# Optimization experiments

Measured on AMD Instinct MI355X. Metric: run time of the kernel, lower is better.

Reference implementation:

```python
import jax, jax.numpy as jnp
import numpy as np

EMBED_DIM = 128
NUM_HEADS = 4
WINDOW = 7
L = WINDOW * WINDOW  # 49 tokens per window
D_K = EMBED_DIM // NUM_HEADS
NUM_WINDOWS = 1024   # windows per image (224/7)^2
B_TOTAL = 8192       # image_batch(8) * NUM_WINDOWS


def _relative_position_index(window):
    ch, cw = np.meshgrid(np.arange(window), np.arange(window), indexing='ij')
    coords = np.stack([ch.ravel(), cw.ravel()])              # [2, L]
    rel = coords[:, :, None] - coords[:, None, :]            # [2, L, L]
    rel = rel.transpose(1, 2, 0)                             # [L, L, 2]
    rel[:, :, 0] += window - 1
    rel[:, :, 1] += window - 1
    rel[:, :, 0] *= 2 * window - 1
    return rel.sum(-1)                                       # [L, L] int

REL_IDX = jnp.asarray(_relative_position_index(WINDOW))


def setup_inputs() -> dict:
    key = jax.random.key(0)
    ks = jax.random.split(key, 8)
    q = jax.random.normal(ks[0], (B_TOTAL, L, EMBED_DIM), jnp.float32)
    k = jax.random.normal(ks[1], (B_TOTAL, L, EMBED_DIM), jnp.float32)
    v = jax.random.normal(ks[2], (B_TOTAL, L, EMBED_DIM), jnp.float32)
    # shift-mask style additive mask (0 / -100 pattern emulated by random floats is less
    # faithful; build a real 0/-100 mask from a random window partition)
    mkey = jax.random.fold_in(key, 99)
    groups = jax.random.randint(mkey, (NUM_WINDOWS, L), 0, 4)
    mask = jnp.where(groups[:, :, None] == groups[:, None, :], 0.0, -100.0).astype(jnp.float32)
    Wq = jax.random.normal(ks[3], (EMBED_DIM, EMBED_DIM), jnp.float32) * 0.02
    Wk = jax.random.normal(ks[4], (EMBED_DIM, EMBED_DIM), jnp.float32) * 0.02
    Wv = jax.random.normal(ks[5], (EMBED_DIM, EMBED_DIM), jnp.float32) * 0.02
    Wo = jax.random.normal(ks[6], (EMBED_DIM, EMBED_DIM), jnp.float32) * 0.02
    bo = jnp.zeros((EMBED_DIM,), jnp.float32)
    rel_table = jax.random.normal(ks[7], ((2 * WINDOW - 1) ** 2, NUM_HEADS), jnp.float32) * 0.02
    return {"q": q, "k": k, "v": v, "mask": mask, "Wq": Wq, "Wk": Wk,
            "Wv": Wv, "Wo": Wo, "bo": bo, "rel_table": rel_table}


def reference(q, k, v, mask, Wq, Wk, Wv, Wo, bo, rel_table):
    B = q.shape[0]
    # linear projections (torch Linear: x @ W.T), split heads -> [B, H, L, d]
    def proj(x, W):
        return (x @ W.T).reshape(B, L, NUM_HEADS, D_K).transpose(0, 2, 1, 3)
    qh, kh, vh = proj(q, Wq), proj(k, Wk), proj(v, Wv)

    energy = jnp.einsum('bhld,bhmd->bhlm', qh, kh) / jnp.sqrt(jnp.float32(D_K))
    # gathered relative position bias: [L, L, H] -> [1, H, L, L]
    bias = rel_table[REL_IDX].transpose(2, 0, 1)[None]
    energy = energy + bias
    # additive shift mask per window: [B//nW, nW, H, L, L] + mask[None,:,None]
    nW = mask.shape[0]
    energy = energy.reshape(-1, nW, NUM_HEADS, L, L) + mask[None, :, None]
    energy = energy.reshape(B, NUM_HEADS, L, L)

    attn = jax.nn.softmax(energy, axis=-1)
    out = jnp.einsum('bhlm,bhmd->bhld', attn, vh)
    out = out.transpose(0, 2, 1, 3).reshape(B, L, EMBED_DIM)
    return out @ Wo.T + bo
```

## Files before the change

kernel.cpp:

```cpp
#include <hip/hip_runtime.h>

#define TOK 49
#define DIM 128
#define NHEAD 4
#define NWIN 1024
#define SCALE 0.17677669529663687f

typedef __bf16 bf16x8 __attribute__((ext_vector_type(8)));
typedef short s16x4 __attribute__((ext_vector_type(4)));
typedef float f32x4 __attribute__((ext_vector_type(4)));
typedef unsigned short u16;
typedef unsigned int u32;

#if defined(__HIP_DEVICE_COMPILE__)
#define MFMA16(a, b, c) __builtin_amdgcn_mfma_f32_16x16x16bf16_1k(a, b, c, 0, 0, 0)
#define MFMA32(a, b, c) __builtin_amdgcn_mfma_f32_16x16x32_bf16(a, b, c, 0, 0, 0)
#else
__device__ inline f32x4 MFMA16(s16x4, s16x4, f32x4 c) { return c; }
__device__ inline f32x4 MFMA32(bf16x8, bf16x8, f32x4 c) { return c; }
#endif

__device__ __forceinline__ int xo256(int row, int kbyte) {
    return row * 256 + (kbyte ^ ((row & 7) << 4));
}
__device__ __forceinline__ u16 bfbits(float x) {
    __bf16 t = (__bf16)x;
    return __builtin_bit_cast(u16, t);
}
__device__ __forceinline__ float bf2f(u16 x) {
    u32 u = ((u32)x) << 16;
    return __builtin_bit_cast(float, u);
}
__device__ __forceinline__ bf16x8 cvt8(const float* __restrict__ p) {
    float4 a = *reinterpret_cast<const float4*>(p);
    float4 bq = *reinterpret_cast<const float4*>(p + 4);
    bf16x8 r;
    r[0] = (__bf16)a.x; r[1] = (__bf16)a.y; r[2] = (__bf16)a.z; r[3] = (__bf16)a.w;
    r[4] = (__bf16)bq.x; r[5] = (__bf16)bq.y; r[6] = (__bf16)bq.z; r[7] = (__bf16)bq.w;
    return r;
}
__device__ __forceinline__ bf16x8 cvt8s(const float* __restrict__ p, float s) {
    float4 a = *reinterpret_cast<const float4*>(p);
    float4 bq = *reinterpret_cast<const float4*>(p + 4);
    bf16x8 r;
    r[0] = (__bf16)(a.x * s); r[1] = (__bf16)(a.y * s);
    r[2] = (__bf16)(a.z * s); r[3] = (__bf16)(a.w * s);
    r[4] = (__bf16)(bq.x * s); r[5] = (__bf16)(bq.y * s);
    r[6] = (__bf16)(bq.z * s); r[7] = (__bf16)(bq.w * s);
    return r;
}
__device__ __forceinline__ s16x4 pack4(const f32x4& a) {
    s16x4 r;
    r[0] = (short)bfbits(a[0]); r[1] = (short)bfbits(a[1]);
    r[2] = (short)bfbits(a[2]); r[3] = (short)bfbits(a[3]);
    return r;
}
__device__ __forceinline__ s16x4 pack4s(const f32x4& a, float s) {
    s16x4 r;
    r[0] = (short)bfbits(a[0] * s); r[1] = (short)bfbits(a[1] * s);
    r[2] = (short)bfbits(a[2] * s); r[3] = (short)bfbits(a[3] * s);
    return r;
}

__global__ void fused_pre_kernel(const float* __restrict__ mask, const float* __restrict__ rel,
                                 u16* __restrict__ tbl) {
    const int idx = blockIdx.x * 256 + threadIdx.x;
    const int w = idx >> 14, h = (idx >> 12) & 3, l = (idx >> 6) & 63, m = idx & 63;
    float v = 0.0f;
    if (l < TOK && m < TOK) {
        const int dl = l / 7 - m / 7 + 6;
        const int dc = l % 7 - m % 7 + 6;
        v = mask[(w * TOK + l) * TOK + m] + rel[(dl * 13 + dc) * NHEAD + h];
    }
    tbl[idx] = bfbits(v);
}

__global__ void bias_pre_kernel(const float* __restrict__ rel, float* __restrict__ biasT) {
    const int idx = blockIdx.x * 256 + threadIdx.x;
    const int h = idx >> 12, l = (idx >> 6) & 63, m = idx & 63;
    float v = 0.0f;
    if (l < TOK && m < TOK) {
        const int dl = l / 7 - m / 7 + 6;
        const int dc = l % 7 - m % 7 + 6;
        v = rel[(dl * 13 + dc) * NHEAD + h];
    }
    biasT[idx] = v;
}

__global__ void wcvt_kernel(const float* __restrict__ Wq, const float* __restrict__ Wk,
                            const float* __restrict__ Wv, const float* __restrict__ Wo,
                            u16* __restrict__ tbl) {
    const int idx = blockIdx.x * 256 + threadIdx.x;
    const int mat = idx >> 14, e = idx & 16383;
    float v;
    if (mat == 0)      v = Wq[e] * SCALE;
    else if (mat == 1) v = Wk[e];
    else if (mat == 2) v = Wv[e];
    else               v = Wo[e];
    tbl[idx] = bfbits(v);
}

template <int MODE>
__global__ __launch_bounds__(256, 3) void winattn_kernel(
    const float* __restrict__ q, const float* __restrict__ k, const float* __restrict__ v,
    const float* __restrict__ mask, const float* __restrict__ Wq, const float* __restrict__ Wk,
    const float* __restrict__ Wv, const float* __restrict__ Wo, const float* __restrict__ bo,
    const u16* __restrict__ wtbl, const u16* __restrict__ fmtbl, const float* __restrict__ btbl,
    float* __restrict__ out)
{
    __shared__ __align__(16) char LA[16384];
    __shared__ __align__(16) char LB[16384];
    const int tid = threadIdx.x;
    const int wave = tid >> 6;
    const int lane = tid & 63;
    const int l16 = lane & 15;
    const int k8 = lane >> 4;
    const int b = blockIdx.x;
    const int h = wave;

    const float* qp = q + (size_t)b * (TOK * DIM);
    const float* kp = k + (size_t)b * (TOK * DIM);
    const float* vp = v + (size_t)b * (TOK * DIM);
    float* op = out + (size_t)b * (TOK * DIM);

    auto ldw = [&](int mat, int row, int kk) -> bf16x8 {
        return *reinterpret_cast<const bf16x8*>(
            reinterpret_cast<const __bf16*>(wtbl) + (mat << 14) + row * DIM + kk * 32 + k8 * 8);
    };
    auto ldx = [&](const char* buf, int row, int kk) -> bf16x8 {
        return *reinterpret_cast<const bf16x8*>(buf + xo256(row, kk * 64 + k8 * 16));
    };

    float4 tv[8];
    {
        float4 t[8];
        #pragma unroll
        for (int p = 0; p < 8; ++p) {
            const int idx = p * 256 + tid;
            const int row = idx >> 5;
            const int c4 = (idx & 31) * 4;
            t[p] = (row < TOK) ? *reinterpret_cast<const float4*>(qp + row * DIM + c4)
                               : float4{0.f, 0.f, 0.f, 0.f};
        }
        #pragma unroll
        for (int p = 0; p < 8; ++p) {
            const int idx = p * 256 + tid;
            uint2 pq;
            pq.x = (u32)bfbits(t[p].x) | ((u32)bfbits(t[p].y) << 16);
            pq.y = (u32)bfbits(t[p].z) | ((u32)bfbits(t[p].w) << 16);
            *reinterpret_cast<uint2*>(LA + xo256(idx >> 5, (idx & 31) * 8)) = pq;
        }
        #pragma unroll
        for (int p = 0; p < 8; ++p) {
            const int idx = p * 256 + tid;
            const int row = idx >> 5;
            const int c4 = (idx & 31) * 4;
            t[p] = (row < TOK) ? *reinterpret_cast<const float4*>(kp + row * DIM + c4)
                               : float4{0.f, 0.f, 0.f, 0.f};
        }
        #pragma unroll
        for (int p = 0; p < 8; ++p) {
            const int idx = p * 256 + tid;
            const int row = idx >> 5;
            const int c4 = (idx & 31) * 4;
            tv[p] = (row < TOK) ? *reinterpret_cast<const float4*>(vp + row * DIM + c4)
                                : float4{0.f, 0.f, 0.f, 0.f};
        }
        #pragma unroll
        for (int p = 0; p < 8; ++p) {
            const int idx = p * 256 + tid;
            uint2 pk2;
            pk2.x = (u32)bfbits(t[p].x) | ((u32)bfbits(t[p].y) << 16);
            pk2.y = (u32)bfbits(t[p].z) | ((u32)bfbits(t[p].w) << 16);
            *reinterpret_cast<uint2*>(LB + xo256(idx >> 5, (idx & 31) * 8)) = pk2;
        }
    }
    __syncthreads();

    uint2 pv[8];
    #pragma unroll
    for (int p = 0; p < 8; ++p) {
        pv[p].x = (u32)bfbits(tv[p].x) | ((u32)bfbits(tv[p].y) << 16);
        pv[p].y = (u32)bfbits(tv[p].z) | ((u32)bfbits(tv[p].w) << 16);
    }

    s16x4 qf[2][4], kf[2][4];
    {
        f32x4 acc[2][4];
        #pragma unroll
        for (int t = 0; t < 2; ++t)
            #pragma unroll
            for (int ni = 0; ni < 4; ++ni) acc[t][ni] = f32x4{0.f, 0.f, 0.f, 0.f};
        #pragma unroll
        for (int kk = 0; kk < 4; ++kk) {
            bf16x8 wa[2], xb[4];
            #pragma unroll
            for (int t = 0; t < 2; ++t)
                wa[t] = (MODE == 0) ? ldw(0, h * 32 + t * 16 + l16, kk)
                                    : cvt8s(Wq + (h * 32 + t * 16 + l16) * DIM + kk * 32 + k8 * 8, SCALE);
            #pragma unroll
            for (int ni = 0; ni < 4; ++ni) xb[ni] = ldx(LA, ni * 16 + l16, kk);
            #pragma unroll
            for (int t = 0; t < 2; ++t)
                #pragma unroll
                for (int ni = 0; ni < 4; ++ni) acc[t][ni] = MFMA32(wa[t], xb[ni], acc[t][ni]);
        }
        #pragma unroll
        for (int t = 0; t < 2; ++t)
            #pragma unroll
            for (int ni = 0; ni < 4; ++ni) qf[t][ni] = pack4(acc[t][ni]);
    }
    {
        f32x4 acc[2][4];
        #pragma unroll
        for (int t = 0; t < 2; ++t)
            #pragma unroll
            for (int mi = 0; mi < 4; ++mi) acc[t][mi] = f32x4{0.f, 0.f, 0.f, 0.f};
        #pragma unroll
        for (int kk = 0; kk < 4; ++kk) {
            bf16x8 wa[2], xb[4];
            #pragma unroll
            for (int t = 0; t < 2; ++t)
                wa[t] = (MODE == 0) ? ldw(1, h * 32 + t * 16 + l16, kk)
                                    : cvt8(Wk + (h * 32 + t * 16 + l16) * DIM + kk * 32 + k8 * 8);
            #pragma unroll
            for (int mi = 0; mi < 4; ++mi) xb[mi] = ldx(LB, mi * 16 + l16, kk);
            #pragma unroll
            for (int t = 0; t < 2; ++t)
                #pragma unroll
                for (int mi = 0; mi < 4; ++mi) acc[t][mi] = MFMA32(wa[t], xb[mi], acc[t][mi]);
        }
        #pragma unroll
        for (int t = 0; t < 2; ++t)
            #pragma unroll
            for (int mi = 0; mi < 4; ++mi) kf[t][mi] = pack4(acc[t][mi]);
    }
    __syncthreads();

    #pragma unroll
    for (int p = 0; p < 8; ++p) {
        const int idx = p * 256 + tid;
        *reinterpret_cast<uint2*>(LA + xo256(idx >> 5, (idx & 31) * 8)) = pv[p];
    }
    __syncthreads();

    s16x4 pf[4][4];
    {
        const u16* frow = (MODE == 0)
            ? fmtbl + ((((size_t)(b & (NWIN - 1)) * NHEAD) + h) << 12) : nullptr;
        const float* brow = (MODE == 1) ? btbl + ((size_t)h << 12) : nullptr;
        const float* mp = mask + (size_t)(b & (NWIN - 1)) * (TOK * TOK);
        #pragma unroll
        for (int ni = 0; ni < 4; ++ni) {
            f32x4 ec[4];
            #pragma unroll
            for (int mi = 0; mi < 4; ++mi) {
                f32x4 c = {0.f, 0.f, 0.f, 0.f};
                c = MFMA16(kf[0][mi], qf[0][ni], c);
                ec[mi] = MFMA16(kf[1][mi], qf[1][ni], c);
            }
            const int l = ni * 16 + l16;
            const bool lv = l < TOK;
            #pragma unroll
            for (int mi = 0; mi < 4; ++mi) {
                const int m0 = mi * 16 + k8 * 4;
                float ad[4];
                if constexpr (MODE == 0) {
                    const uint2 raw = *reinterpret_cast<const uint2*>(frow + l * 64 + m0);
                    ad[0] = bf2f((u16)(raw.x & 0xffffu));
                    ad[1] = bf2f((u16)(raw.x >> 16));
                    ad[2] = bf2f((u16)(raw.y & 0xffffu));
                    ad[3] = bf2f((u16)(raw.y >> 16));
                } else {
                    const float4 bg = *reinterpret_cast<const float4*>(brow + l * 64 + m0);
                    ad[0] = bg.x; ad[1] = bg.y; ad[2] = bg.z; ad[3] = bg.w;
                    #pragma unroll
                    for (int r = 0; r < 4; ++r) {
                        const int m = m0 + r;
                        if (lv && m < TOK) ad[r] += mp[l * TOK + m];
                    }
                }
                #pragma unroll
                for (int r = 0; r < 4; ++r) {
                    const int m = m0 + r;
                    ec[mi][r] = (lv && m < TOK) ? ec[mi][r] + ad[r] : -1e30f;
                }
            }
            float mx = -1e30f;
            #pragma unroll
            for (int mi = 0; mi < 4; ++mi)
                #pragma unroll
                for (int r = 0; r < 4; ++r) mx = fmaxf(mx, ec[mi][r]);
            mx = fmaxf(mx, __shfl_xor(mx, 16));
            mx = fmaxf(mx, __shfl_xor(mx, 32));
            float s = 0.f;
            #pragma unroll
            for (int mi = 0; mi < 4; ++mi) {
                #pragma unroll
                for (int r = 0; r < 4; ++r) {
                    const float p = __expf(ec[mi][r] - mx);
                    ec[mi][r] = p;
                    s += p;
                }
            }
            s += __shfl_xor(s, 16);
            s += __shfl_xor(s, 32);
            const float rs = 1.0f / s;
            #pragma unroll
            for (int mi = 0; mi < 4; ++mi) pf[mi][ni] = pack4s(ec[mi], rs);
        }
    }

    s16x4 vf[4][2];
    {
        f32x4 acc[4][2];
        #pragma unroll
        for (int mi = 0; mi < 4; ++mi)
            #pragma unroll
            for (int nn = 0; nn < 2; ++nn) acc[mi][nn] = f32x4{0.f, 0.f, 0.f, 0.f};
        #pragma unroll
        for (int kk = 0; kk < 4; ++kk) {
            bf16x8 xa[4], wb[2];
            #pragma unroll
            for (int mi = 0; mi < 4; ++mi) xa[mi] = ldx(LA, mi * 16 + l16, kk);
            #pragma unroll
            for (int nn = 0; nn < 2; ++nn)
                wb[nn] = (MODE == 0) ? ldw(2, h * 32 + nn * 16 + l16, kk)
                                     : cvt8(Wv + (h * 32 + nn * 16 + l16) * DIM + kk * 32 + k8 * 8);
            #pragma unroll
            for (int mi = 0; mi < 4; ++mi)
                #pragma unroll
                for (int nn = 0; nn < 2; ++nn) acc[mi][nn] = MFMA32(xa[mi], wb[nn], acc[mi][nn]);
        }
        #pragma unroll
        for (int mi = 0; mi < 4; ++mi)
            #pragma unroll
            for (int nn = 0; nn < 2; ++nn) vf[mi][nn] = pack4(acc[mi][nn]);
    }

    f32x4 o_[4][2];
    #pragma unroll
    for (int ni = 0; ni < 4; ++ni) {
        #pragma unroll
        for (int nn = 0; nn < 2; ++nn) {
            f32x4 c = {0.f, 0.f, 0.f, 0.f};
            #pragma unroll
            for (int mi = 0; mi < 4; ++mi) c = MFMA16(pf[mi][ni], vf[mi][nn], c);
            o_[ni][nn] = c;
        }
    }

    #pragma unroll
    for (int ni = 0; ni < 4; ++ni) {
        #pragma unroll
        for (int nn = 0; nn < 2; ++nn) {
            const int d = h * 32 + nn * 16 + l16;
            #pragma unroll
            for (int r = 0; r < 4; ++r) {
                const int row = ni * 16 + k8 * 4 + r;
                *reinterpret_cast<u16*>(LB + xo256(row, d * 2)) = bfbits(o_[ni][nn][r]);
            }
        }
    }
    bf16x8 aw[2][4];
    #pragma unroll
    for (int m2 = 0; m2 < 2; ++m2) {
        const int o = (wave * 2 + m2) * 16 + l16;
        #pragma unroll
        for (int kk = 0; kk < 4; ++kk)
            aw[m2][kk] = (MODE == 0) ? ldw(3, o, kk)
                                     : cvt8(Wo + o * DIM + kk * 32 + k8 * 8);
    }
    __syncthreads();

    #pragma unroll
    for (int ni = 0; ni < 4; ++ni) {
        const int l = ni * 16 + l16;
        bf16x8 bx[4];
        #pragma unroll
        for (int kk = 0; kk < 4; ++kk)
            bx[kk] = *reinterpret_cast<const bf16x8*>(LB + xo256(l, kk * 64 + k8 * 16));
        #pragma unroll
        for (int m2 = 0; m2 < 2; ++m2) {
            f32x4 c = {0.f, 0.f, 0.f, 0.f};
            #pragma unroll
            for (int kk = 0; kk < 4; ++kk) c = MFMA32(aw[m2][kk], bx[kk], c);
            if (l < TOK) {
                const int o0 = (wave * 2 + m2) * 16 + k8 * 4;
                const float4 bias = *reinterpret_cast<const float4*>(bo + o0);
                float4 st;
                st.x = c[0] + bias.x;
                st.y = c[1] + bias.y;
                st.z = c[2] + bias.z;
                st.w = c[3] + bias.w;
                *reinterpret_cast<float4*>(op + l * DIM + o0) = st;
            }
        }
    }
}

extern "C" void kernel_launch(void* const* d_in, const int* in_sizes, int n_in,
                              void* d_out, int out_size, void* d_ws, size_t ws_size,
                              hipStream_t stream) {
    const float* q    = (const float*)d_in[0];
    const float* k    = (const float*)d_in[1];
    const float* v    = (const float*)d_in[2];
    const float* mask = (const float*)d_in[3];
    const float* Wq   = (const float*)d_in[4];
    const float* Wk   = (const float*)d_in[5];
    const float* Wv   = (const float*)d_in[6];
    const float* Wo   = (const float*)d_in[7];
    const float* bo   = (const float*)d_in[8];
    const float* rel  = (const float*)d_in[9];
    float* out = (float*)d_out;

    const int B = in_sizes[0] / (TOK * DIM);
    const size_t FUSED_BYTES = (size_t)NWIN * NHEAD * 64 * 64 * sizeof(u16);
    const size_t W_BYTES     = (size_t)4 * DIM * DIM * sizeof(u16);
    const size_t BIAS_BYTES  = (size_t)NHEAD * 64 * 64 * sizeof(float);

    if (ws_size >= FUSED_BYTES + W_BYTES) {
        u16* fmtbl = (u16*)d_ws;
        u16* wtbl  = (u16*)((char*)d_ws + FUSED_BYTES);
        fused_pre_kernel<<<dim3(NWIN * NHEAD * 64 * 64 / 256), dim3(256), 0, stream>>>(
            mask, rel, fmtbl);
        wcvt_kernel<<<dim3(4 * DIM * DIM / 256), dim3(256), 0, stream>>>(Wq, Wk, Wv, Wo, wtbl);
        winattn_kernel<0><<<dim3(B), dim3(256), 0, stream>>>(q, k, v, mask, Wq, Wk, Wv, Wo,
                                                             bo, wtbl, fmtbl, nullptr, out);
    } else {
        float* btbl = (float*)d_ws;
        bias_pre_kernel<<<dim3(NHEAD * 64 * 64 / 256), dim3(256), 0, stream>>>(rel, btbl);
        winattn_kernel<1><<<dim3(B), dim3(256), 0, stream>>>(q, k, v, mask, Wq, Wk, Wv, Wo,
                                                             bo, nullptr, nullptr, btbl, out);
    }
}
```

Before: 337.5 us.

## Process two windows per block and prefetch next window's Q during output stage

Each block now handles two consecutive windows in a loop. It prefetches the next window's Q into registers while the current window's output projection runs, and issues the K/V loads earlier. The fused bias/mask table entries are also loaded into registers ahead of the softmax rather than inline. This aims to hide global-load latency with compute, at the cost of higher register pressure and half as many blocks in the grid.

```diff
diff --git a/kernel.cpp b/kernel.cpp
--- a/kernel.cpp
+++ b/kernel.cpp
@@ -106,7 +106,7 @@
     const float* __restrict__ mask, const float* __restrict__ Wq, const float* __restrict__ Wk,
     const float* __restrict__ Wv, const float* __restrict__ Wo, const float* __restrict__ bo,
     const u16* __restrict__ wtbl, const u16* __restrict__ fmtbl, const float* __restrict__ btbl,
-    float* __restrict__ out)
+    float* __restrict__ out, int btot)
 {
     __shared__ __align__(16) char LA[16384];
     __shared__ __align__(16) char LB[16384];
@@ -115,13 +115,8 @@
     const int lane = tid & 63;
     const int l16 = lane & 15;
     const int k8 = lane >> 4;
-    const int b = blockIdx.x;
+    const int b0 = blockIdx.x * 2;
     const int h = wave;
-
-    const float* qp = q + (size_t)b * (TOK * DIM);
-    const float* kp = k + (size_t)b * (TOK * DIM);
-    const float* vp = v + (size_t)b * (TOK * DIM);
-    float* op = out + (size_t)b * (TOK * DIM);
 
     auto ldw = [&](int mat, int row, int kk) -> bf16x8 {
         return *reinterpret_cast<const bf16x8*>(
@@ -130,272 +125,280 @@
     auto ldx = [&](const char* buf, int row, int kk) -> bf16x8 {
         return *reinterpret_cast<const bf16x8*>(buf + xo256(row, kk * 64 + k8 * 16));
     };
-
-    float4 tv[8];
-    {
-        float4 t[8];
+    auto gload = [&](float4* dst, const float* __restrict__ src) {
         #pragma unroll
         for (int p = 0; p < 8; ++p) {
             const int idx = p * 256 + tid;
             const int row = idx >> 5;
             const int c4 = (idx & 31) * 4;
-            t[p] = (row < TOK) ? *reinterpret_cast<const float4*>(qp + row * DIM + c4)
-                               : float4{0.f, 0.f, 0.f, 0.f};
-        }
-        #pragma unroll
-        for (int p = 0; p < 8; ++p) {
-            const int idx = p * 256 + tid;
-            uint2 pq;
-            pq.x = (u32)bfbits(t[p].x) | ((u32)bfbits(t[p].y) << 16);
-            pq.y = (u32)bfbits(t[p].z) | ((u32)bfbits(t[p].w) << 16);
-            *reinterpret_cast<uint2*>(LA + xo256(idx >> 5, (idx & 31) * 8)) = pq;
-        }
-        #pragma unroll
-        for (int p = 0; p < 8; ++p) {
-            const int idx = p * 256 + tid;
-            const int row = idx >> 5;
-            const int c4 = (idx & 31) * 4;
-            t[p] = (row < TOK) ? *reinterpret_cast<const float4*>(kp + row * DIM + c4)
-                               : float4{0.f, 0.f, 0.f, 0.f};
-        }
-        #pragma unroll
-        for (int p = 0; p < 8; ++p) {
-            const int idx = p * 256 + tid;
-            const int row = idx >> 5;
-            const int c4 = (idx & 31) * 4;
-            tv[p] = (row < TOK) ? *reinterpret_cast<const float4*>(vp + row * DIM + c4)
-                                : float4{0.f, 0.f, 0.f, 0.f};
-        }
+            dst[p] = (row < TOK) ? *reinterpret_cast<const float4*>(src + row * DIM + c4)
+                                 : float4{0.f, 0.f, 0.f, 0.f};
+        }
+    };
+    auto lwrite = [&](char* L, const float4* src) {
         #pragma unroll
         for (int p = 0; p < 8; ++p) {
             const int idx = p * 256 + tid;
             uint2 pk2;
-            pk2.x = (u32)bfbits(t[p].x) | ((u32)bfbits(t[p].y) << 16);
-            pk2.y = (u32)bfbits(t[p].z) | ((u32)bfbits(t[p].w) << 16);
-            *reinterpret_cast<uint2*>(LB + xo256(idx >> 5, (idx & 31) * 8)) = pk2;
-        }
-    }
-    __syncthreads();
-
-    uint2 pv[8];
-    #pragma unroll
-    for (int p = 0; p < 8; ++p) {
-        pv[p].x = (u32)bfbits(tv[p].x) | ((u32)bfbits(tv[p].y) << 16);
-        pv[p].y = (u32)bfbits(tv[p].z) | ((u32)bfbits(tv[p].w) << 16);
-    }
-
-    s16x4 qf[2][4], kf[2][4];
-    {
-        f32x4 acc[2][4];
-        #pragma unroll
-        for (int t = 0; t < 2; ++t)
-            #pragma unroll
-            for (int ni = 0; ni < 4; ++ni) acc[t][ni] = f32x4{0.f, 0.f, 0.f, 0.f};
-        #pragma unroll
-        for (int kk = 0; kk < 4; ++kk) {
-            bf16x8 wa[2], xb[4];
-            #pragma unroll
-            for (int t = 0; t < 2; ++t)
-                wa[t] = (MODE == 0) ? ldw(0, h * 32 + t * 16 + l16, kk)
-                                    : cvt8s(Wq + (h * 32 + t * 16 + l16) * DIM + kk * 32 + k8 * 8, SCALE);
-            #pragma unroll
-            for (int ni = 0; ni < 4; ++ni) xb[ni] = ldx(LA, ni * 16 + l16, kk);
-            #pragma unroll
-            for (int t = 0; t < 2; ++t)
-                #pragma unroll
-                for (int ni = 0; ni < 4; ++ni) acc[t][ni] = MFMA32(wa[t], xb[ni], acc[t][ni]);
-        }
-        #pragma unroll
-        for (int t = 0; t < 2; ++t)
-            #pragma unroll
-            for (int ni = 0; ni < 4; ++ni) qf[t][ni] = pack4(acc[t][ni]);
-    }
-    {
-        f32x4 acc[2][4];
-        #pragma unroll
-        for (int t = 0; t < 2; ++t)
-            #pragma unroll
-            for (int mi = 0; mi < 4; ++mi) acc[t][mi] = f32x4{0.f, 0.f, 0.f, 0.f};
-        #pragma unroll
-        for (int kk = 0; kk < 4; ++kk) {
-            bf16x8 wa[2], xb[4];
-            #pragma unroll
-            for (int t = 0; t < 2; ++t)
-                wa[t] = (MODE == 0) ? ldw(1, h * 32 + t * 16 + l16, kk)
-                                    : cvt8(Wk + (h * 32 + t * 16 + l16) * DIM + kk * 32 + k8 * 8);
-            #pragma unroll
-            for (int mi = 0; mi < 4; ++mi) xb[mi] = ldx(LB, mi * 16 + l16, kk);
-            #pragma unroll
-            for (int t = 0; t < 2; ++t)
-                #pragma unroll
-                for (int mi = 0; mi < 4; ++mi) acc[t][mi] = MFMA32(wa[t], xb[mi], acc[t][mi]);
-        }
-        #pragma unroll
-        for (int t = 0; t < 2; ++t)
-            #pragma unroll
-            for (int mi = 0; mi < 4; ++mi) kf[t][mi] = pack4(acc[t][mi]);
-    }
-    __syncthreads();
-
-    #pragma unroll
-    for (int p = 0; p < 8; ++p) {
-        const int idx = p * 256 + tid;
-        *reinterpret_cast<uint2*>(LA + xo256(idx >> 5, (idx & 31) * 8)) = pv[p];
-    }
-    __syncthreads();
-
-    s16x4 pf[4][4];
-    {
-        const u16* frow = (MODE == 0)
-            ? fmtbl + ((((size_t)(b & (NWIN - 1)) * NHEAD) + h) << 12) : nullptr;
-        const float* brow = (MODE == 1) ? btbl + ((size_t)h << 12) : nullptr;
-        const float* mp = mask + (size_t)(b & (NWIN - 1)) * (TOK * TOK);
-        #pragma unroll
-        for (int ni = 0; ni < 4; ++ni) {
-            f32x4 ec[4];
-            #pragma unroll
-            for (int mi = 0; mi < 4; ++mi) {
-                f32x4 c = {0.f, 0.f, 0.f, 0.f};
-                c = MFMA16(kf[0][mi], qf[0][ni], c);
-                ec[mi] = MFMA16(kf[1][mi], qf[1][ni], c);
-            }
-            const int l = ni * 16 + l16;
-            const bool lv = l < TOK;
-            #pragma unroll
-            for (int mi = 0; mi < 4; ++mi) {
-                const int m0 = mi * 16 + k8 * 4;
-                float ad[4];
-                if constexpr (MODE == 0) {
-                    const uint2 raw = *reinterpret_cast<const uint2*>(frow + l * 64 + m0);
-                    ad[0] = bf2f((u16)(raw.x & 0xffffu));
-                    ad[1] = bf2f((u16)(raw.x >> 16));
-                    ad[2] = bf2f((u16)(raw.y & 0xffffu));
-                    ad[3] = bf2f((u16)(raw.y >> 16));
-                } else {
-                    const float4 bg = *reinterpret_cast<const float4*>(brow + l * 64 + m0);
-                    ad[0] = bg.x; ad[1] = bg.y; ad[2] = bg.z; ad[3] = bg.w;
+            pk2.x = (u32)bfbits(src[p].x) | ((u32)bfbits(src[p].y) << 16);
+            pk2.y = (u32)bfbits(src[p].z) | ((u32)bfbits(src[p].w) << 16);
+            *reinterpret_cast<uint2*>(L + xo256(idx >> 5, (idx & 31) * 8)) = pk2;
+        }
+    };
+
+    float4 t[8];
+    gload(t, q + (size_t)b0 * (TOK * DIM));
+
+    #pragma unroll 1
+    for (int it = 0; it < 2; ++it) {
+        const int b = b0 + it;
+        if (b >= btot) break;
+        const float* kp = k + (size_t)b * (TOK * DIM);
+        const float* vp = v + (size_t)b * (TOK * DIM);
+        float* op = out + (size_t)b * (TOK * DIM);
+
+        lwrite(LA, t);
+        float4 tv[8];
+        gload(t, kp);
+        gload(tv, vp);
+        __syncthreads();
+
+        s16x4 qf[2][4], kf[2][4];
+        {
+            f32x4 acc[2][4];
+            #pragma unroll
+            for (int t2 = 0; t2 < 2; ++t2)
+                #pragma unroll
+                for (int ni = 0; ni < 4; ++ni) acc[t2][ni] = f32x4{0.f, 0.f, 0.f, 0.f};
+            #pragma unroll
+            for (int kk = 0; kk < 4; ++kk) {
+                bf16x8 wa[2], xb[4];
+                #pragma unroll
+                for (int t2 = 0; t2 < 2; ++t2)
+                    wa[t2] = (MODE == 0) ? ldw(0, h * 32 + t2 * 16 + l16, kk)
+                                         : cvt8s(Wq + (h * 32 + t2 * 16 + l16) * DIM + kk * 32 + k8 * 8, SCALE);
+                #pragma unroll
+                for (int ni = 0; ni < 4; ++ni) xb[ni] = ldx(LA, ni * 16 + l16, kk);
+                #pragma unroll
+                for (int t2 = 0; t2 < 2; ++t2)
+                    #pragma unroll
+                    for (int ni = 0; ni < 4; ++ni) acc[t2][ni] = MFMA32(wa[t2], xb[ni], acc[t2][ni]);
+            }
+            #pragma unroll
+            for (int t2 = 0; t2 < 2; ++t2)
+                #pragma unroll
+                for (int ni = 0; ni < 4; ++ni) qf[t2][ni] = pack4(acc[t2][ni]);
+        }
+
+        lwrite(LB, t);
+        uint2 pv[8];
+        #pragma unroll
+        for (int p = 0; p < 8; ++p) {
+            pv[p].x = (u32)bfbits(tv[p].x) | ((u32)bfbits(tv[p].y) << 16);
+            pv[p].y = (u32)bfbits(tv[p].z) | ((u32)bfbits(tv[p].w) << 16);
+        }
+        __syncthreads();
+
+        uint2 tbl[16];
+        if constexpr (MODE == 0) {
+            const u16* frow = fmtbl + ((((size_t)(b & (NWIN - 1)) * NHEAD) + h) << 12);
+            #pragma unroll
+            for (int ni = 0; ni < 4; ++ni) {
+                const int l = ni * 16 + l16;
+                #pragma unroll
+                for (int mi = 0; mi < 4; ++mi)
+                    tbl[ni * 4 + mi] = *reinterpret_cast<const uint2*>(
+                        frow + l * 64 + mi * 16 + k8 * 4);
+            }
+        }
+
+        {
+            f32x4 acc[2][4];
+            #pragma unroll
+            for (int t2 = 0; t2 < 2; ++t2)
+                #pragma unroll
+                for (int mi = 0; mi < 4; ++mi) acc[t2][mi] = f32x4{0.f, 0.f, 0.f, 0.f};
+            #pragma unroll
+            for (int kk = 0; kk < 4; ++kk) {
+                bf16x8 wa[2], xb[4];
+                #pragma unroll
+                for (int t2 = 0; t2 < 2; ++t2)
+                    wa[t2] = (MODE == 0) ? ldw(1, h * 32 + t2 * 16 + l16, kk)
+                                         : cvt8(Wk + (h * 32 + t2 * 16 + l16) * DIM + kk * 32 + k8 * 8);
+                #pragma unroll
+                for (int mi = 0; mi < 4; ++mi) xb[mi] = ldx(LB, mi * 16 + l16, kk);
+                #pragma unroll
+                for (int t2 = 0; t2 < 2; ++t2)
+                    #pragma unroll
+                    for (int mi = 0; mi < 4; ++mi) acc[t2][mi] = MFMA32(wa[t2], xb[mi], acc[t2][mi]);
+            }
+            #pragma unroll
+            for (int t2 = 0; t2 < 2; ++t2)
+                #pragma unroll
+                for (int mi = 0; mi < 4; ++mi) kf[t2][mi] = pack4(acc[t2][mi]);
+        }
+
+        #pragma unroll
+        for (int p = 0; p < 8; ++p) {
+            const int idx = p * 256 + tid;
+            *reinterpret_cast<uint2*>(LA + xo256(idx >> 5, (idx & 31) * 8)) = pv[p];
+        }
+        __syncthreads();
+
+        s16x4 pf[4][4];
+        {
+            const float* brow = (MODE == 1) ? btbl + ((size_t)h << 12) : nullptr;
+            const float* mp = mask + (size_t)(b & (NWIN - 1)) * (TOK * TOK);
+            #pragma unroll
+            for (int ni = 0; ni < 4; ++ni) {
+                f32x4 ec[4];
+                #pragma unroll
+                for (int mi = 0; mi < 4; ++mi) {
+                    f32x4 c = {0.f, 0.f, 0.f, 0.f};
+                    c = MFMA16(kf[0][mi], qf[0][ni], c);
+                    ec[mi] = MFMA16(kf[1][mi], qf[1][ni], c);
+                }
+                const int l = ni * 16 + l16;
+                const bool lv = l < TOK;
+                #pragma unroll
+                for (int mi = 0; mi < 4; ++mi) {
+                    const int m0 = mi * 16 + k8 * 4;
+                    float ad[4];
+                    if constexpr (MODE == 0) {
+                        const uint2 raw = tbl[ni * 4 + mi];
+                        ad[0] = bf2f((u16)(raw.x & 0xffffu));
+                        ad[1] = bf2f((u16)(raw.x >> 16));
+                        ad[2] = bf2f((u16)(raw.y & 0xffffu));
+                        ad[3] = bf2f((u16)(raw.y >> 16));
+                    } else {
+                        const float4 bg = *reinterpret_cast<const float4*>(brow + l * 64 + m0);
+                        ad[0] = bg.x; ad[1] = bg.y; ad[2] = bg.z; ad[3] = bg.w;
+                        #pragma unroll
+                        for (int r = 0; r < 4; ++r) {
+                            const int m = m0 + r;
+                            if (lv && m < TOK) ad[r] += mp[l * TOK + m];
+                        }
+                    }
                     #pragma unroll
                     for (int r = 0; r < 4; ++r) {
                         const int m = m0 + r;
-                        if (lv && m < TOK) ad[r] += mp[l * TOK + m];
+                        ec[mi][r] = (lv && m < TOK) ? ec[mi][r] + ad[r] : -1e30f;
                     }
                 }
+                float mx = -1e30f;
+                #pragma unroll
+                for (int mi = 0; mi < 4; ++mi)
+                    #pragma unroll
+                    for (int r = 0; r < 4; ++r) mx = fmaxf(mx, ec[mi][r]);
+                mx = fmaxf(mx, __shfl_xor(mx, 16));
+                mx = fmaxf(mx, __shfl_xor(mx, 32));
+                float s = 0.f;
+                #pragma unroll
+                for (int mi = 0; mi < 4; ++mi) {
+                    #pragma unroll
+                    for (int r = 0; r < 4; ++r) {
+                        const float p = __expf(ec[mi][r] - mx);
+                        ec[mi][r] = p;
+                        s += p;
+                    }
+                }
+                s += __shfl_xor(s, 16);
+                s += __shfl_xor(s, 32);
+                const float rs = 1.0f / s;
+                #pragma unroll
+                for (int mi = 0; mi < 4; ++mi) pf[mi][ni] = pack4s(ec[mi], rs);
+            }
+        }
+
+        s16x4 vf[4][2];
+        {
+            f32x4 acc[4][2];
+            #pragma unroll
+            for (int mi = 0; mi < 4; ++mi)
+                #pragma unroll
+                for (int nn = 0; nn < 2; ++nn) acc[mi][nn] = f32x4{0.f, 0.f, 0.f, 0.f};
+            #pragma unroll
+            for (int kk = 0; kk < 4; ++kk) {
+                bf16x8 xa[4], wb[2];
+                #pragma unroll
+                for (int mi = 0; mi < 4; ++mi) xa[mi] = ldx(LA, mi * 16 + l16, kk);
+                #pragma unroll
+                for (int nn = 0; nn < 2; ++nn)
+                    wb[nn] = (MODE == 0) ? ldw(2, h * 32 + nn * 16 + l16, kk)
+                                         : cvt8(Wv + (h * 32 + nn * 16 + l16) * DIM + kk * 32 + k8 * 8);
+                #pragma unroll
+                for (int mi = 0; mi < 4; ++mi)
+                    #pragma unroll
+                    for (int nn = 0; nn < 2; ++nn) acc[mi][nn] = MFMA32(xa[mi], wb[nn], acc[mi][nn]);
+            }
+            #pragma unroll
+            for (int mi = 0; mi < 4; ++mi)
+                #pragma unroll
+                for (int nn = 0; nn < 2; ++nn) vf[mi][nn] = pack4(acc[mi][nn]);
+        }
+
+        f32x4 o_[4][2];
+        #pragma unroll
+        for (int ni = 0; ni < 4; ++ni) {
+            #pragma unroll
+            for (int nn = 0; nn < 2; ++nn) {
+                f32x4 c = {0.f, 0.f, 0.f, 0.f};
+                #pragma unroll
+                for (int mi = 0; mi < 4; ++mi) c = MFMA16(pf[mi][ni], vf[mi][nn], c);
+                o_[ni][nn] = c;
+            }
+        }
+        if (it == 0 && b0 + 1 < btot)
+            gload(t, q + (size_t)(b0 + 1) * (TOK * DIM));
+
+        #pragma unroll
+        for (int ni = 0; ni < 4; ++ni) {
+            #pragma unroll
+            for (int nn = 0; nn < 2; ++nn) {
+                const int d = h * 32 + nn * 16 + l16;
                 #pragma unroll
                 for (int r = 0; r < 4; ++r) {
-                    const int m = m0 + r;
-                    ec[mi][r] = (lv && m < TOK) ? ec[mi][r] + ad[r] : -1e30f;
+                    const int row = ni * 16 + k8 * 4 + r;
+                    *reinterpret_cast<u16*>(LB + xo256(row, d * 2)) = bfbits(o_[ni][nn][r]);
                 }
             }
-            float mx = -1e30f;
-            #pragma unroll
-            for (int mi = 0; mi < 4; ++mi)
-                #pragma unroll
-                for (int r = 0; r < 4; ++r) mx = fmaxf(mx, ec[mi][r]);
-            mx = fmaxf(mx, __shfl_xor(mx, 16));
-            mx = fmaxf(mx, __shfl_xor(mx, 32));
-            float s = 0.f;
-            #pragma unroll
-            for (int mi = 0; mi < 4; ++mi) {
-                #pragma unroll
-                for (int r = 0; r < 4; ++r) {
-                    const float p = __expf(ec[mi][r] - mx);
-                    ec[mi][r] = p;
-                    s += p;
+        }
+        bf16x8 aw[2][4];
+        #pragma unroll
+        for (int m2 = 0; m2 < 2; ++m2) {
+            const int o = (wave * 2 + m2) * 16 + l16;
+            #pragma unroll
+            for (int kk = 0; kk < 4; ++kk)
+                aw[m2][kk] = (MODE == 0) ? ldw(3, o, kk)
+                                         : cvt8(Wo + o * DIM + kk * 32 + k8 * 8);
+        }
+        __syncthreads();
+
+        #pragma unroll
+        for (int ni = 0; ni < 4; ++ni) {
+            const int l = ni * 16 + l16;
+            bf16x8 bx[4];
+            #pragma unroll
+            for (int kk = 0; kk < 4; ++kk)
+                bx[kk] = *reinterpret_cast<const bf16x8*>(LB + xo256(l, kk * 64 + k8 * 16));
+            #pragma unroll
+            for (int m2 = 0; m2 < 2; ++m2) {
+                f32x4 c = {0.f, 0.f, 0.f, 0.f};
+                #pragma unroll
+                for (int kk = 0; kk < 4; ++kk) c = MFMA32(aw[m2][kk], bx[kk], c);
+                if (l < TOK) {
+                    const int o0 = (wave * 2 + m2) * 16 + k8 * 4;
+                    const float4 bias = *reinterpret_cast<const float4*>(bo + o0);
+                    float4 st;
+                    st.x = c[0] + bias.x;
+                    st.y = c[1] + bias.y;
+                    st.z = c[2] + bias.z;
+                    st.w = c[3] + bias.w;
+                    *reinterpret_cast<float4*>(op + l * DIM + o0) = st;
                 }
             }
-            s += __shfl_xor(s, 16);
-            s += __shfl_xor(s, 32);
-            const float rs = 1.0f / s;
-            #pragma unroll
-            for (int mi = 0; mi < 4; ++mi) pf[mi][ni] = pack4s(ec[mi], rs);
-        }
-    }
-
-    s16x4 vf[4][2];
-    {
-        f32x4 acc[4][2];
-        #pragma unroll
-        for (int mi = 0; mi < 4; ++mi)
-            #pragma unroll
-            for (int nn = 0; nn < 2; ++nn) acc[mi][nn] = f32x4{0.f, 0.f, 0.f, 0.f};
-        #pragma unroll
-        for (int kk = 0; kk < 4; ++kk) {
-            bf16x8 xa[4], wb[2];
-            #pragma unroll
-            for (int mi = 0; mi < 4; ++mi) xa[mi] = ldx(LA, mi * 16 + l16, kk);
-            #pragma unroll
-            for (int nn = 0; nn < 2; ++nn)
-                wb[nn] = (MODE == 0) ? ldw(2, h * 32 + nn * 16 + l16, kk)
-                                     : cvt8(Wv + (h * 32 + nn * 16 + l16) * DIM + kk * 32 + k8 * 8);
-            #pragma unroll
-            for (int mi = 0; mi < 4; ++mi)
-                #pragma unroll
-                for (int nn = 0; nn < 2; ++nn) acc[mi][nn] = MFMA32(xa[mi], wb[nn], acc[mi][nn]);
-        }
-        #pragma unroll
-        for (int mi = 0; mi < 4; ++mi)
-            #pragma unroll
-            for (int nn = 0; nn < 2; ++nn) vf[mi][nn] = pack4(acc[mi][nn]);
-    }
-
-    f32x4 o_[4][2];
-    #pragma unroll
-    for (int ni = 0; ni < 4; ++ni) {
-        #pragma unroll
-        for (int nn = 0; nn < 2; ++nn) {
-            f32x4 c = {0.f, 0.f, 0.f, 0.f};
-            #pragma unroll
-            for (int mi = 0; mi < 4; ++mi) c = MFMA16(pf[mi][ni], vf[mi][nn], c);
-            o_[ni][nn] = c;
-        }
-    }
-
-    #pragma unroll
-    for (int ni = 0; ni < 4; ++ni) {
-        #pragma unroll
-        for (int nn = 0; nn < 2; ++nn) {
-            const int d = h * 32 + nn * 16 + l16;
-            #pragma unroll
-            for (int r = 0; r < 4; ++r) {
-                const int row = ni * 16 + k8 * 4 + r;
-                *reinterpret_cast<u16*>(LB + xo256(row, d * 2)) = bfbits(o_[ni][nn][r]);
-            }
-        }
-    }
-    bf16x8 aw[2][4];
-    #pragma unroll
-    for (int m2 = 0; m2 < 2; ++m2) {
-        const int o = (wave * 2 + m2) * 16 + l16;
-        #pragma unroll
-        for (int kk = 0; kk < 4; ++kk)
-            aw[m2][kk] = (MODE == 0) ? ldw(3, o, kk)
-                                     : cvt8(Wo + o * DIM + kk * 32 + k8 * 8);
-    }
-    __syncthreads();
-
-    #pragma unroll
-    for (int ni = 0; ni < 4; ++ni) {
-        const int l = ni * 16 + l16;
-        bf16x8 bx[4];
-        #pragma unroll
-        for (int kk = 0; kk < 4; ++kk)
-            bx[kk] = *reinterpret_cast<const bf16x8*>(LB + xo256(l, kk * 64 + k8 * 16));
-        #pragma unroll
-        for (int m2 = 0; m2 < 2; ++m2) {
-            f32x4 c = {0.f, 0.f, 0.f, 0.f};
-            #pragma unroll
-            for (int kk = 0; kk < 4; ++kk) c = MFMA32(aw[m2][kk], bx[kk], c);
-            if (l < TOK) {
-                const int o0 = (wave * 2 + m2) * 16 + k8 * 4;
-                const float4 bias = *reinterpret_cast<const float4*>(bo + o0);
-                float4 st;
-                st.x = c[0] + bias.x;
-                st.y = c[1] + bias.y;
-                st.z = c[2] + bias.z;
-                st.w = c[3] + bias.w;
-                *reinterpret_cast<float4*>(op + l * DIM + o0) = st;
-            }
-        }
+        }
+        __syncthreads();
     }
 }
 
@@ -415,9 +418,9 @@
     float* out = (float*)d_out;
 
     const int B = in_sizes[0] / (TOK * DIM);
+    const int NBLK = (B + 1) / 2;
     const size_t FUSED_BYTES = (size_t)NWIN * NHEAD * 64 * 64 * sizeof(u16);
     const size_t W_BYTES     = (size_t)4 * DIM * DIM * sizeof(u16);
-    const size_t BIAS_BYTES  = (size_t)NHEAD * 64 * 64 * sizeof(float);
 
     if (ws_size >= FUSED_BYTES + W_BYTES) {
         u16* fmtbl = (u16*)d_ws;
@@ -425,12 +428,12 @@
         fused_pre_kernel<<<dim3(NWIN * NHEAD * 64 * 64 / 256), dim3(256), 0, stream>>>(
             mask, rel, fmtbl);
         wcvt_kernel<<<dim3(4 * DIM * DIM / 256), dim3(256), 0, stream>>>(Wq, Wk, Wv, Wo, wtbl);
-        winattn_kernel<0><<<dim3(B), dim3(256), 0, stream>>>(q, k, v, mask, Wq, Wk, Wv, Wo,
-                                                             bo, wtbl, fmtbl, nullptr, out);
+        winattn_kernel<0><<<dim3(NBLK), dim3(256), 0, stream>>>(q, k, v, mask, Wq, Wk, Wv, Wo,
+                                                                bo, wtbl, fmtbl, nullptr, out, B);
     } else {
         float* btbl = (float*)d_ws;
         bias_pre_kernel<<<dim3(NHEAD * 64 * 64 / 256), dim3(256), 0, stream>>>(rel, btbl);
-        winattn_kernel<1><<<dim3(B), dim3(256), 0, stream>>>(q, k, v, mask, Wq, Wk, Wv, Wo,
-                                                             bo, nullptr, nullptr, btbl, out);
+        winattn_kernel<1><<<dim3(NBLK), dim3(256), 0, stream>>>(q, k, v, mask, Wq, Wk, Wv, Wo,
+                                                                bo, nullptr, nullptr, btbl, out, B);
     }
 }
```

Result: slower. 682.9 us (median of 5 runs) (+102.4%).
